# Performance work log

Hardware: AMD Instinct MI355X
Metric: run time of the kernel (lower is better)

## Reference

```python
import jax, jax.numpy as jnp
import numpy as np

EPS = 1e-6

def _rmsnorm(x, w):
    # normalize over last (head_dim) axis
    return x * jax.lax.rsqrt(jnp.mean(x * x, axis=-1, keepdims=True) + EPS) * w

def _rope(x, cos, sin):
    # x: [B, H, S, D]; cos/sin: [S, D]
    d = x.shape[-1]
    x1, x2 = x[..., : d // 2], x[..., d // 2 :]
    rot = jnp.concatenate([-x2, x1], axis=-1)
    return x * cos[None, None] + rot * sin[None, None]

def setup_inputs() -> dict:
    key = jax.random.key(0)
    B, S, D_MODEL = 1, 2048, 2048
    HEADS, HEAD_DIM, NKV = 32, 64, 8
    d_out = HEADS * HEAD_DIM
    kv_d_out = NKV * HEAD_DIM
    ks = jax.random.split(key, 8)
    x = jax.random.normal(ks[0], (B, S, D_MODEL), dtype=jnp.float32)
    # RoPE tables
    inv_freq = 1.0 / (10000.0 ** (jnp.arange(0, HEAD_DIM, 2, dtype=jnp.float32) / HEAD_DIM))
    pos = jnp.arange(S, dtype=jnp.float32)
    ang = pos[:, None] * inv_freq[None, :]            # [S, D/2]
    ang = jnp.concatenate([ang, ang], axis=-1)        # [S, D]
    sin, cos = jnp.sin(ang), jnp.cos(ang)
    mask = jnp.tril(jnp.ones((S, S), dtype=bool))     # causal: True = attend
    sd = 0.02
    Wq = jax.random.normal(ks[1], (D_MODEL, d_out), dtype=jnp.float32) * sd
    Wk = jax.random.normal(ks[2], (D_MODEL, kv_d_out), dtype=jnp.float32) * sd
    Wv = jax.random.normal(ks[3], (D_MODEL, kv_d_out), dtype=jnp.float32) * sd
    Wo = jax.random.normal(ks[4], (d_out, D_MODEL), dtype=jnp.float32) * sd
    bo = jnp.zeros((D_MODEL,), dtype=jnp.float32)
    q_scale = jnp.ones((HEAD_DIM,), dtype=jnp.float32)
    k_scale = jnp.ones((HEAD_DIM,), dtype=jnp.float32)
    return {"x": x, "sin": sin, "cos": cos, "mask": mask, "Wq": Wq, "Wk": Wk,
            "Wv": Wv, "Wo": Wo, "bo": bo, "q_scale": q_scale, "k_scale": k_scale}

def reference(x, sin, cos, mask, Wq, Wk, Wv, Wo, bo, q_scale, k_scale):
    B, S, _ = x.shape
    HEADS, HEAD_DIM, NKV = 32, 64, 8
    GS = HEADS // NKV  # group size = 4
    q = (x @ Wq).reshape(B, S, HEADS, HEAD_DIM).transpose(0, 2, 1, 3)  # [B,H,S,D]
    k = (x @ Wk).reshape(B, S, NKV, HEAD_DIM).transpose(0, 2, 1, 3)    # [B,G,S,D]
    v = (x @ Wv).reshape(B, S, NKV, HEAD_DIM).transpose(0, 2, 1, 3)    # [B,G,S,D]
    q = _rmsnorm(q, q_scale)
    k = _rmsnorm(k, k_scale)
    q = _rope(q, cos, sin)
    k = _rope(k, cos, sin)
    # GQA without materializing repeated k/v: group query heads per kv group
    qg = q.reshape(B, NKV, GS, S, HEAD_DIM)
    scale = 1.0 / jnp.sqrt(jnp.asarray(HEAD_DIM, dtype=x.dtype))
    scores = jnp.einsum('bghqd,bgkd->bghqk', qg, k) * scale  # [B,G,Gs,S,S]
    scores = jnp.where(mask[None, None, None], scores, jnp.asarray(-jnp.inf, dtype=scores.dtype))
    attn = jax.nn.softmax(scores, axis=-1)
    out = jnp.einsum('bghqk,bgkd->bghqd', attn, v)            # [B,G,Gs,S,D]
    out = out.reshape(B, HEADS, S, HEAD_DIM).transpose(0, 2, 1, 3).reshape(B, S, HEADS * HEAD_DIM)
    return out @ Wo + bo
```

## Files before the change

### kernel.cpp

```cpp
#include <hip/hip_runtime.h>
#include <stdint.h>


typedef __bf16 bf16x8 __attribute__((ext_vector_type(8)));
typedef __bf16 bf16x4v __attribute__((ext_vector_type(4)));
typedef float f32x4 __attribute__((ext_vector_type(4)));

#define MFMA_BF16(a, b, c) __builtin_amdgcn_mfma_f32_16x16x32_bf16(a, b, c, 0, 0, 0)

#if __has_builtin(__builtin_amdgcn_exp2f)
#define EXP2F(x) __builtin_amdgcn_exp2f(x)
#else
#define EXP2F(x) __expf((x) * 0.69314718055994531f)
#endif

#define QSCALE 0.18033688011112042f
#define SHIFT2 11.541560327111707f

__device__ __forceinline__ unsigned short f2bf(float f) {
  unsigned int u = __float_as_uint(f);
  u += 0x7fffu + ((u >> 16) & 1u);
  return (unsigned short)(u >> 16);
}

__device__ __forceinline__ void gload_lds16(const unsigned short* gsrc,
                                            unsigned short* ldst) {
  __builtin_amdgcn_global_load_lds(
      (const __attribute__((address_space(1))) unsigned int*)gsrc,
      (__attribute__((address_space(3))) unsigned int*)ldst, 16, 0, 0);
}

__global__ __launch_bounds__(256) void transpose_all(const float* __restrict__ Wq,
                                                     const float* __restrict__ Wk,
                                                     const float* __restrict__ Wv,
                                                     const float* __restrict__ Wo,
                                                     const float* __restrict__ x,
                                                     unsigned short* __restrict__ Wqkvt,
                                                     unsigned short* __restrict__ Wot,
                                                     unsigned short* __restrict__ xb) {
  int bx = blockIdx.x;
  int tid = threadIdx.x;
  if (bx >= 80) {
    int bid = (bx - 80) * 32 + blockIdx.y;
#pragma unroll
    for (int p = 0; p < 8; p++) {
      int i = bid * 8192 + p * 1024 + tid * 4;
      float4 v = *(const float4*)&x[i];
      ushort4 o;
      o.x = f2bf(v.x); o.y = f2bf(v.y); o.z = f2bf(v.z); o.w = f2bf(v.w);
      *(ushort4*)&xb[i] = o;
    }
    return;
  }
  const float* W;
  unsigned short* T;
  int N, nb;
  if (bx < 32)      { W = Wq; T = Wqkvt;                       N = 2048; nb = bx * 64; }
  else if (bx < 40) { W = Wk; T = Wqkvt + 2048 * 2048;         N = 512;  nb = (bx - 32) * 64; }
  else if (bx < 48) { W = Wv; T = Wqkvt + (size_t)2560 * 2048; N = 512;  nb = (bx - 40) * 64; }
  else              { W = Wo; T = Wot;                         N = 2048; nb = (bx - 48) * 64; }
  int kb = blockIdx.y * 64;
  __shared__ float tile[64][65];
#pragma unroll
  for (int i = 0; i < 16; i++) {
    int idx = tid + i * 256;
    int r = idx >> 6, c = idx & 63;
    tile[r][c] = W[(size_t)(kb + r) * N + nb + c];
  }
  __syncthreads();
#pragma unroll
  for (int i = 0; i < 8; i++) {
    int idx = tid + i * 256;
    int r = idx >> 5, cp = idx & 31;
    ushort2 o;
    o.x = f2bf(tile[2 * cp][r]);
    o.y = f2bf(tile[2 * cp + 1][r]);
    *(ushort2*)&T[(size_t)(nb + r) * 2048 + kb + 2 * cp] = o;
  }
}

#define GEMM_DBUF(A_, B_, m0_, n0_)                                            \
  int quad = lane >> 4, l16 = lane & 15;                                       \
  int wrow = (w & 1) * 32, wcol = (w >> 1) * 64;                               \
  int rsub = lane >> 3, csub = lane & 7;                                       \
  int chunk = csub ^ rsub;                                                     \
  int slotL = quad ^ (l16 & 7);                                                \
  const unsigned short* gA = &A_[(size_t)(m0_ + w * 16 + rsub) * 2048 + chunk * 8]; \
  const unsigned short* gB = &B_[(size_t)(n0_ + w * 32 + rsub) * 2048 + chunk * 8]; \
  int laOff = (w * 16) * 64 + lane * 8;                                        \
  int lbOff = 64 * 64 + (w * 32) * 64 + lane * 8;                              \
  f32x4 acc[2][4];                                                             \
  _Pragma("unroll") for (int i = 0; i < 2; i++)                                \
      _Pragma("unroll") for (int j = 0; j < 4; j++)                            \
          acc[i][j] = (f32x4){0.f, 0.f, 0.f, 0.f};                             \
  {                                                                            \
    unsigned short* sp = &Stage[0][0];                                         \
    gload_lds16(gA, sp + laOff);                                               \
    gload_lds16(gA + 8 * 2048, sp + laOff + 8 * 64);                           \
    gload_lds16(gB, sp + lbOff);                                               \
    gload_lds16(gB + 8 * 2048, sp + lbOff + 8 * 64);                           \
    gload_lds16(gB + 16 * 2048, sp + lbOff + 16 * 64);                         \
    gload_lds16(gB + 24 * 2048, sp + lbOff + 24 * 64);                         \
  }                                                                            \
  for (int k0 = 0; k0 < 2048; k0 += 64) {                                      \
    __syncthreads();                                                           \
    unsigned short* cur = &Stage[(k0 >> 6) & 1][0];                            \
    unsigned short* nxt = &Stage[((k0 >> 6) + 1) & 1][0];                      \
    if (k0 + 64 < 2048) {                                                      \
      int kn = k0 + 64;                                                        \
      gload_lds16(gA + kn, nxt + laOff);                                       \
      gload_lds16(gA + 8 * 2048 + kn, nxt + laOff + 8 * 64);                   \
      gload_lds16(gB + kn, nxt + lbOff);                                       \
      gload_lds16(gB + 8 * 2048 + kn, nxt + lbOff + 8 * 64);                   \
      gload_lds16(gB + 16 * 2048 + kn, nxt + lbOff + 16 * 64);                 \
      gload_lds16(gB + 24 * 2048 + kn, nxt + lbOff + 24 * 64);                 \
    }                                                                          \
    const unsigned short* As = cur;                                            \
    const unsigned short* Bs = cur + 64 * 64;                                  \
    bf16x8 af[2][2], bfr[4][2];                                                \
    _Pragma("unroll") for (int i = 0; i < 2; i++) {                            \
      int base = (wrow + i * 16 + l16) * 64;                                   \
      af[i][0] = *(const bf16x8*)&As[base + slotL * 8];                        \
      af[i][1] = *(const bf16x8*)&As[base + (slotL ^ 4) * 8];                  \
    }                                                                          \
    _Pragma("unroll") for (int j = 0; j < 4; j++) {                            \
      int base = (wcol + j * 16 + l16) * 64;                                   \
      bfr[j][0] = *(const bf16x8*)&Bs[base + slotL * 8];                       \
      bfr[j][1] = *(const bf16x8*)&Bs[base + (slotL ^ 4) * 8];                 \
    }                                                                          \
    _Pragma("unroll") for (int kc = 0; kc < 2; kc++)                           \
        _Pragma("unroll") for (int i = 0; i < 2; i++)                          \
            _Pragma("unroll") for (int j = 0; j < 4; j++)                      \
                acc[i][j] = MFMA_BF16(af[i][kc], bfr[j][kc], acc[i][j]);       \
  }

__global__ __launch_bounds__(256, 3) void gemm_qkv(const unsigned short* __restrict__ A,
                                                   const unsigned short* __restrict__ B,
                                                   const float* __restrict__ sinp,
                                                   const float* __restrict__ cosp,
                                                   const float* __restrict__ q_scale,
                                                   const float* __restrict__ k_scale,
                                                   unsigned short* __restrict__ qh,
                                                   unsigned short* __restrict__ kh,
                                                   unsigned short* __restrict__ vt) {
  __shared__ __align__(16) unsigned short Stage[2][192 * 64];
  int tid = threadIdx.x;
  int w = tid >> 6, lane = tid & 63;
  int m0 = blockIdx.y * 64;
  int n0 = blockIdx.x * 128;
  GEMM_DBUF(A, B, m0, n0)

  int hd = blockIdx.x * 2 + (w >> 1);
  if (hd < 40) {
    const float* scl = (hd < 32) ? q_scale : k_scale;
    float wsc[4];
#pragma unroll
    for (int j = 0; j < 4; j++) wsc[j] = scl[j * 16 + l16];
    float oscale = (hd < 32) ? QSCALE : 1.0f;
#pragma unroll
    for (int i = 0; i < 2; i++)
#pragma unroll
      for (int r = 0; r < 4; r++) {
        float ss = 0.f;
#pragma unroll
        for (int j = 0; j < 4; j++) ss += acc[i][j][r] * acc[i][j][r];
#pragma unroll
        for (int off = 8; off; off >>= 1) ss += __shfl_xor(ss, off);
        float inv = rsqrtf(ss * (1.f / 64.f) + 1e-6f);
        int s = m0 + wrow + i * 16 + quad * 4 + r;
        float xn[4];
#pragma unroll
        for (int j = 0; j < 4; j++) xn[j] = acc[i][j][r] * inv * wsc[j];
#pragma unroll
        for (int j = 0; j < 4; j++) {
          int d = j * 16 + l16;
          float rot = (j < 2) ? -xn[j + 2] : xn[j - 2];
          float out = (xn[j] * cosp[s * 64 + d] + rot * sinp[s * 64 + d]) * oscale;
          if (hd < 32) qh[(size_t)s * 2048 + hd * 64 + d] = f2bf(out);
          else         kh[(size_t)s * 512 + (hd - 32) * 64 + d] = f2bf(out);
        }
      }
  } else {
    int g = hd - 40;
#pragma unroll
    for (int i = 0; i < 2; i++) {
      int t = (wrow + i * 16) >> 4;
      int slotb = (t & 1) * 32 + quad * 8 + (t >> 1) * 4;
#pragma unroll
      for (int j = 0; j < 4; j++) {
        bf16x4v pk;
#pragma unroll
        for (int r = 0; r < 4; r++) pk[r] = (__bf16)acc[i][j][r];
        *(bf16x4v*)&vt[(size_t)(g * 64 + j * 16 + l16) * 2048 + m0 + slotb] = pk;
      }
    }
  }
}

__global__ __launch_bounds__(256, 3) void gemm_out(const unsigned short* __restrict__ A,
                                                   const unsigned short* __restrict__ B,
                                                   float* __restrict__ C,
                                                   const float* __restrict__ bias) {
  __shared__ __align__(16) unsigned short Stage[2][192 * 64];
  int tid = threadIdx.x;
  int w = tid >> 6, lane = tid & 63;
  int m0 = blockIdx.y * 64;
  int n0 = blockIdx.x * 128;
  GEMM_DBUF(A, B, m0, n0)

#pragma unroll
  for (int i = 0; i < 2; i++) {
    int row = m0 + wrow + i * 16 + quad * 4;
#pragma unroll
    for (int j = 0; j < 4; j++) {
      int col = n0 + wcol + j * 16 + l16;
      float b = bias[col];
#pragma unroll
      for (int r = 0; r < 4; r++)
        C[(size_t)(row + r) * 2048 + col] = acc[i][j][r] + b;
    }
  }
}

__global__ __launch_bounds__(256, 4) void attention(const unsigned short* __restrict__ qh,
                                                    const unsigned short* __restrict__ kh,
                                                    const unsigned short* __restrict__ vt,
                                                    unsigned short* __restrict__ aout) {
  int h = blockIdx.y;
  int g = h >> 2;
  int tile = (blockIdx.x + blockIdx.y) & 31;
  int q0 = tile * 64;
  int w = threadIdx.x >> 6;
  int lane = threadIdx.x & 63;
  int quad = lane >> 4;
  int l16 = lane & 15;
  int qrow0 = q0 + w * 16;

  __shared__ __align__(16) unsigned short Stage[8192];
  unsigned short* Ks = Stage;
  unsigned short* Vs = Stage + 4096;

  int rsub = lane >> 3;
  int csub = lane & 7;
  int chunk = csub ^ rsub;

  const unsigned short* kg = &kh[(size_t)(w * 16 + rsub) * 512 + g * 64 + chunk * 8];
  const unsigned short* vg = &vt[(size_t)(g * 64 + w * 16 + rsub) * 2048 + chunk * 8];
  unsigned short* kl = Ks + (w * 16) * 64 + lane * 8;
  unsigned short* vl = Vs + (w * 16) * 64 + lane * 8;

  int posL = quad ^ (l16 & 7);
  int fL = l16 * 64 + posL * 8;
  int fH = l16 * 64 + (posL ^ 4) * 8;

  bf16x8 bq0 = *(const bf16x8*)&qh[(size_t)(qrow0 + l16) * 2048 + h * 64 + quad * 8];
  bf16x8 bq1 = *(const bf16x8*)&qh[(size_t)(qrow0 + l16) * 2048 + h * 64 + 32 + quad * 8];

  f32x4 o[4];
#pragma unroll
  for (int j = 0; j < 4; j++) o[j] = (f32x4){0.f, 0.f, 0.f, 0.f};
  float l_run = 0.f;

  int T = tile + 1;
  for (int it = 0; it < T; ++it) {
    int n0 = it << 6;
    __syncthreads();
    gload_lds16(kg + (size_t)n0 * 512, kl);
    gload_lds16(kg + (size_t)(n0 + 8) * 512, kl + 8 * 64);
    gload_lds16(vg + n0, vl);
    gload_lds16(vg + n0 + 8 * 2048, vl + 8 * 64);
    __syncthreads();

    f32x4 s[4];
#pragma unroll
    for (int t = 0; t < 4; ++t) {
      bf16x8 kfl = *(const bf16x8*)&Ks[t * 1024 + fL];
      bf16x8 kfh = *(const bf16x8*)&Ks[t * 1024 + fH];
      f32x4 zz = (f32x4){0.f, 0.f, 0.f, 0.f};
      zz = MFMA_BF16(kfl, bq0, zz);
      s[t] = MFMA_BF16(kfh, bq1, zz);
    }

    float pv[4][4];
    if (it == T - 1) {
      int qg = qrow0 + l16;
#pragma unroll
      for (int t = 0; t < 4; ++t)
#pragma unroll
        for (int r = 0; r < 4; ++r) {
          int key = n0 + t * 16 + quad * 4 + r;
          float p = (key <= qg) ? EXP2F(s[t][r] - SHIFT2) : 0.f;
          l_run += p;
          pv[t][r] = p;
        }
    } else {
#pragma unroll
      for (int t = 0; t < 4; ++t)
#pragma unroll
        for (int r = 0; r < 4; ++r) {
          float p = EXP2F(s[t][r] - SHIFT2);
          l_run += p;
          pv[t][r] = p;
        }
    }

    bf16x8 pf0, pf1;
#pragma unroll
    for (int j = 0; j < 4; ++j) {
      pf0[j] = (__bf16)pv[0][j];
      pf0[j + 4] = (__bf16)pv[2][j];
      pf1[j] = (__bf16)pv[1][j];
      pf1[j + 4] = (__bf16)pv[3][j];
    }

#pragma unroll
    for (int jd = 0; jd < 4; ++jd) {
      bf16x8 vfl = *(const bf16x8*)&Vs[jd * 1024 + fL];
      bf16x8 vfh = *(const bf16x8*)&Vs[jd * 1024 + fH];
      o[jd] = MFMA_BF16(vfl, pf0, o[jd]);
      o[jd] = MFMA_BF16(vfh, pf1, o[jd]);
    }
  }

  l_run += __shfl_xor(l_run, 16);
  l_run += __shfl_xor(l_run, 32);
  float linv = 1.f / l_run;

  __syncthreads();
  unsigned short* Ob = Stage + w * (16 * 68);
#pragma unroll
  for (int jd = 0; jd < 4; ++jd) {
    bf16x4v pk;
#pragma unroll
    for (int r = 0; r < 4; ++r) pk[r] = (__bf16)(o[jd][r] * linv);
    *(bf16x4v*)&Ob[l16 * 68 + jd * 16 + quad * 4] = pk;
  }
  __threadfence_block();
#pragma unroll
  for (int rr = 0; rr < 2; ++rr) {
    int cidx = rr * 64 + lane;
    int row = cidx >> 3, ch = cidx & 7;
    bf16x8 v = *(const bf16x8*)&Ob[row * 68 + ch * 8];
    *(bf16x8*)&aout[(size_t)(qrow0 + row) * 2048 + h * 64 + ch * 8] = v;
  }
}

extern "C" void kernel_launch(void* const* d_in, const int* in_sizes, int n_in,
                              void* d_out, int out_size, void* d_ws, size_t ws_size,
                              hipStream_t stream) {
  (void)in_sizes; (void)n_in; (void)out_size; (void)ws_size;
  const float* x    = (const float*)d_in[0];
  const float* sinp = (const float*)d_in[1];
  const float* cosp = (const float*)d_in[2];
  const float* Wq = (const float*)d_in[4];
  const float* Wk = (const float*)d_in[5];
  const float* Wv = (const float*)d_in[6];
  const float* Wo = (const float*)d_in[7];
  const float* bo = (const float*)d_in[8];
  const float* q_scale = (const float*)d_in[9];
  const float* k_scale = (const float*)d_in[10];
  float* outp = (float*)d_out;

  uint8_t* ws = (uint8_t*)d_ws;
  const size_t MB = 1024 * 1024;
  unsigned short* xb    = (unsigned short*)(ws);
  unsigned short* Wqkvt = (unsigned short*)(ws + 8 * MB);
  unsigned short* Wot   = (unsigned short*)(ws + 20 * MB);
  unsigned short* qh    = (unsigned short*)(ws + 28 * MB);
  unsigned short* kh    = (unsigned short*)(ws + 36 * MB);
  unsigned short* vt    = (unsigned short*)(ws + 38 * MB);
  unsigned short* aout  = (unsigned short*)(ws + 40 * MB);

  transpose_all<<<dim3(96, 32), 256, 0, stream>>>(Wq, Wk, Wv, Wo, x, Wqkvt, Wot, xb);
  gemm_qkv<<<dim3(24, 32), 256, 0, stream>>>(xb, Wqkvt, sinp, cosp, q_scale, k_scale,
                                             qh, kh, vt);
  attention<<<dim3(32, 32), 256, 0, stream>>>(qh, kh, vt, aout);
  gemm_out<<<dim3(16, 32), 256, 0, stream>>>(aout, Wot, outp, bo);
}
```

Before: 213.1 us.

## Enlarge GEMM tiles to 128x128 per block with 64x64 per-wave subtiles

Both projection GEMMs now use a 128x128 output tile per block instead of 64x128, and each wave computes a 64x64 subtile with a 4x4 MFMA accumulator array. Loading is reorganised so waves 0-1 stage A rows and waves 2-3 stage B rows, eight 16-byte loads each, and the grid is swapped so blockIdx.x walks M. This raises arithmetic intensity per LDS byte and per global load. In exchange the grid has fewer blocks (384 and 256) for the chip's CUs, more registers and LDS are used, and launch bounds drop to 2 blocks per CU.

```diff
diff --git a/kernel.cpp b/kernel.cpp
--- a/kernel.cpp
+++ b/kernel.cpp
@@ -79,62 +79,47 @@
   }
 }
 
-#define GEMM_DBUF(A_, B_, m0_, n0_)                                            \
+#define GEMM_CORE128(A_, B_, m0_, n0_)                                         \
   int quad = lane >> 4, l16 = lane & 15;                                       \
-  int wrow = (w & 1) * 32, wcol = (w >> 1) * 64;                               \
+  int wrow = (w & 1) * 64, wcol = (w >> 1) * 64;                               \
   int rsub = lane >> 3, csub = lane & 7;                                       \
   int chunk = csub ^ rsub;                                                     \
   int slotL = quad ^ (l16 & 7);                                                \
-  const unsigned short* gA = &A_[(size_t)(m0_ + w * 16 + rsub) * 2048 + chunk * 8]; \
-  const unsigned short* gB = &B_[(size_t)(n0_ + w * 32 + rsub) * 2048 + chunk * 8]; \
-  int laOff = (w * 16) * 64 + lane * 8;                                        \
-  int lbOff = 64 * 64 + (w * 32) * 64 + lane * 8;                              \
-  f32x4 acc[2][4];                                                             \
-  _Pragma("unroll") for (int i = 0; i < 2; i++)                                \
+  const unsigned short* gS = (w < 2)                                           \
+      ? &A_[(size_t)(m0_ + w * 64 + rsub) * 2048 + chunk * 8]                  \
+      : &B_[(size_t)(n0_ + (w - 2) * 64 + rsub) * 2048 + chunk * 8];           \
+  int lsOff = (w * 64) * 64 + lane * 8;                                        \
+  f32x4 acc[4][4];                                                             \
+  _Pragma("unroll") for (int i = 0; i < 4; i++)                                \
       _Pragma("unroll") for (int j = 0; j < 4; j++)                            \
           acc[i][j] = (f32x4){0.f, 0.f, 0.f, 0.f};                             \
-  {                                                                            \
-    unsigned short* sp = &Stage[0][0];                                         \
-    gload_lds16(gA, sp + laOff);                                               \
-    gload_lds16(gA + 8 * 2048, sp + laOff + 8 * 64);                           \
-    gload_lds16(gB, sp + lbOff);                                               \
-    gload_lds16(gB + 8 * 2048, sp + lbOff + 8 * 64);                           \
-    gload_lds16(gB + 16 * 2048, sp + lbOff + 16 * 64);                         \
-    gload_lds16(gB + 24 * 2048, sp + lbOff + 24 * 64);                         \
-  }                                                                            \
+  _Pragma("unroll") for (int c = 0; c < 8; c++)                                \
+      gload_lds16(gS + (size_t)c * 8 * 2048, &Stage[0][0] + lsOff + c * 8 * 64); \
   for (int k0 = 0; k0 < 2048; k0 += 64) {                                      \
     __syncthreads();                                                           \
-    unsigned short* cur = &Stage[(k0 >> 6) & 1][0];                            \
+    const unsigned short* cur = &Stage[(k0 >> 6) & 1][0];                      \
     unsigned short* nxt = &Stage[((k0 >> 6) + 1) & 1][0];                      \
     if (k0 + 64 < 2048) {                                                      \
-      int kn = k0 + 64;                                                        \
-      gload_lds16(gA + kn, nxt + laOff);                                       \
-      gload_lds16(gA + 8 * 2048 + kn, nxt + laOff + 8 * 64);                   \
-      gload_lds16(gB + kn, nxt + lbOff);                                       \
-      gload_lds16(gB + 8 * 2048 + kn, nxt + lbOff + 8 * 64);                   \
-      gload_lds16(gB + 16 * 2048 + kn, nxt + lbOff + 16 * 64);                 \
-      gload_lds16(gB + 24 * 2048 + kn, nxt + lbOff + 24 * 64);                 \
+      _Pragma("unroll") for (int c = 0; c < 8; c++)                            \
+          gload_lds16(gS + (size_t)c * 8 * 2048 + k0 + 64,                     \
+                      nxt + lsOff + c * 8 * 64);                               \
     }                                                                          \
     const unsigned short* As = cur;                                            \
-    const unsigned short* Bs = cur + 64 * 64;                                  \
-    bf16x8 af[2][2], bfr[4][2];                                                \
-    _Pragma("unroll") for (int i = 0; i < 2; i++) {                            \
-      int base = (wrow + i * 16 + l16) * 64;                                   \
-      af[i][0] = *(const bf16x8*)&As[base + slotL * 8];                        \
-      af[i][1] = *(const bf16x8*)&As[base + (slotL ^ 4) * 8];                  \
+    const unsigned short* Bs = cur + 128 * 64;                                 \
+    _Pragma("unroll") for (int kc = 0; kc < 2; kc++) {                         \
+      int sl = (kc == 0) ? slotL : (slotL ^ 4);                                \
+      bf16x8 af[4], bfr[4];                                                    \
+      _Pragma("unroll") for (int i = 0; i < 4; i++)                            \
+          af[i] = *(const bf16x8*)&As[(wrow + i * 16 + l16) * 64 + sl * 8];    \
+      _Pragma("unroll") for (int j = 0; j < 4; j++)                            \
+          bfr[j] = *(const bf16x8*)&Bs[(wcol + j * 16 + l16) * 64 + sl * 8];   \
+      _Pragma("unroll") for (int i = 0; i < 4; i++)                            \
+          _Pragma("unroll") for (int j = 0; j < 4; j++)                        \
+              acc[i][j] = MFMA_BF16(af[i], bfr[j], acc[i][j]);                 \
     }                                                                          \
-    _Pragma("unroll") for (int j = 0; j < 4; j++) {                            \
-      int base = (wcol + j * 16 + l16) * 64;                                   \
-      bfr[j][0] = *(const bf16x8*)&Bs[base + slotL * 8];                       \
-      bfr[j][1] = *(const bf16x8*)&Bs[base + (slotL ^ 4) * 8];                 \
-    }                                                                          \
-    _Pragma("unroll") for (int kc = 0; kc < 2; kc++)                           \
-        _Pragma("unroll") for (int i = 0; i < 2; i++)                          \
-            _Pragma("unroll") for (int j = 0; j < 4; j++)                      \
-                acc[i][j] = MFMA_BF16(af[i][kc], bfr[j][kc], acc[i][j]);       \
-  }
-
-__global__ __launch_bounds__(256, 3) void gemm_qkv(const unsigned short* __restrict__ A,
+  }
+
+__global__ __launch_bounds__(256, 2) void gemm_qkv(const unsigned short* __restrict__ A,
                                                    const unsigned short* __restrict__ B,
                                                    const float* __restrict__ sinp,
                                                    const float* __restrict__ cosp,
@@ -143,14 +128,14 @@
                                                    unsigned short* __restrict__ qh,
                                                    unsigned short* __restrict__ kh,
                                                    unsigned short* __restrict__ vt) {
-  __shared__ __align__(16) unsigned short Stage[2][192 * 64];
+  __shared__ __align__(16) unsigned short Stage[2][256 * 64];
   int tid = threadIdx.x;
   int w = tid >> 6, lane = tid & 63;
-  int m0 = blockIdx.y * 64;
-  int n0 = blockIdx.x * 128;
-  GEMM_DBUF(A, B, m0, n0)
-
-  int hd = blockIdx.x * 2 + (w >> 1);
+  int m0 = blockIdx.x * 128;
+  int n0 = blockIdx.y * 128;
+  GEMM_CORE128(A, B, m0, n0)
+
+  int hd = blockIdx.y * 2 + (w >> 1);
   if (hd < 40) {
     const float* scl = (hd < 32) ? q_scale : k_scale;
     float wsc[4];
@@ -158,7 +143,7 @@
     for (int j = 0; j < 4; j++) wsc[j] = scl[j * 16 + l16];
     float oscale = (hd < 32) ? QSCALE : 1.0f;
 #pragma unroll
-    for (int i = 0; i < 2; i++)
+    for (int i = 0; i < 4; i++)
 #pragma unroll
       for (int r = 0; r < 4; r++) {
         float ss = 0.f;
@@ -182,34 +167,34 @@
       }
   } else {
     int g = hd - 40;
-#pragma unroll
-    for (int i = 0; i < 2; i++) {
-      int t = (wrow + i * 16) >> 4;
-      int slotb = (t & 1) * 32 + quad * 8 + (t >> 1) * 4;
+    int base = m0 + (w & 1) * 64;
+#pragma unroll
+    for (int i = 0; i < 4; i++) {
+      int slotb = (i & 1) * 32 + quad * 8 + (i >> 1) * 4;
 #pragma unroll
       for (int j = 0; j < 4; j++) {
         bf16x4v pk;
 #pragma unroll
         for (int r = 0; r < 4; r++) pk[r] = (__bf16)acc[i][j][r];
-        *(bf16x4v*)&vt[(size_t)(g * 64 + j * 16 + l16) * 2048 + m0 + slotb] = pk;
+        *(bf16x4v*)&vt[(size_t)(g * 64 + j * 16 + l16) * 2048 + base + slotb] = pk;
       }
     }
   }
 }
 
-__global__ __launch_bounds__(256, 3) void gemm_out(const unsigned short* __restrict__ A,
+__global__ __launch_bounds__(256, 2) void gemm_out(const unsigned short* __restrict__ A,
                                                    const unsigned short* __restrict__ B,
                                                    float* __restrict__ C,
                                                    const float* __restrict__ bias) {
-  __shared__ __align__(16) unsigned short Stage[2][192 * 64];
+  __shared__ __align__(16) unsigned short Stage[2][256 * 64];
   int tid = threadIdx.x;
   int w = tid >> 6, lane = tid & 63;
-  int m0 = blockIdx.y * 64;
-  int n0 = blockIdx.x * 128;
-  GEMM_DBUF(A, B, m0, n0)
-
-#pragma unroll
-  for (int i = 0; i < 2; i++) {
+  int m0 = blockIdx.x * 128;
+  int n0 = blockIdx.y * 128;
+  GEMM_CORE128(A, B, m0, n0)
+
+#pragma unroll
+  for (int i = 0; i < 4; i++) {
     int row = m0 + wrow + i * 16 + quad * 4;
 #pragma unroll
     for (int j = 0; j < 4; j++) {
@@ -372,8 +357,8 @@
   unsigned short* aout  = (unsigned short*)(ws + 40 * MB);
 
   transpose_all<<<dim3(96, 32), 256, 0, stream>>>(Wq, Wk, Wv, Wo, x, Wqkvt, Wot, xb);
-  gemm_qkv<<<dim3(24, 32), 256, 0, stream>>>(xb, Wqkvt, sinp, cosp, q_scale, k_scale,
+  gemm_qkv<<<dim3(16, 24), 256, 0, stream>>>(xb, Wqkvt, sinp, cosp, q_scale, k_scale,
                                              qh, kh, vt);
   attention<<<dim3(32, 32), 256, 0, stream>>>(qh, kh, vt, aout);
-  gemm_out<<<dim3(16, 32), 256, 0, stream>>>(aout, Wot, outp, bo);
-}
+  gemm_out<<<dim3(16, 16), 256, 0, stream>>>(aout, Wot, outp, bo);
+}
```

After: 218.1 us. 2.4% more time.
